# Kernel tuning notes

Hardware: AMD Instinct MI355X
Metric: run time of the kernel (lower is better)

## Reference

```python
import jax, jax.numpy as jnp
import numpy as np

EMBED_DIM = 1024
NUM_HEADS = 16
HEAD_DIM = EMBED_DIM // NUM_HEADS


def setup_inputs() -> dict:
    key = jax.random.key(0)
    ks = jax.random.split(key, 10)
    s = 1.0 / np.sqrt(EMBED_DIM)
    inp = {
        "x1": jax.random.normal(ks[0], (4, 1024, EMBED_DIM), jnp.float32),
        "x2": jax.random.normal(ks[1], (4, 2048, EMBED_DIM), jnp.float32),
        "Wq": jax.random.normal(ks[2], (EMBED_DIM, EMBED_DIM), jnp.float32) * s,
        "bq": jnp.zeros((EMBED_DIM,), jnp.float32),
        "Wk": jax.random.normal(ks[3], (EMBED_DIM, EMBED_DIM), jnp.float32) * s,
        "bk": jnp.zeros((EMBED_DIM,), jnp.float32),
        "Wv": jax.random.normal(ks[4], (EMBED_DIM, EMBED_DIM), jnp.float32) * s,
        "bv": jnp.zeros((EMBED_DIM,), jnp.float32),
        "Wo": jax.random.normal(ks[5], (EMBED_DIM, EMBED_DIM), jnp.float32) * s,
        "bo": jnp.zeros((EMBED_DIM,), jnp.float32),
    }
    return inp


def reference(x1, x2, Wq, bq, Wk, bk, Wv, bv, Wo, bo):
    B, Sq, E = x1.shape
    Skv = x2.shape[1]
    H, D = NUM_HEADS, HEAD_DIM
    # linear projections (PyTorch Linear: x @ W.T + b)
    q = (x1 @ Wq.T + bq).reshape(B, Sq, H, D).transpose(0, 2, 1, 3)   # [B,H,Sq,D]
    k = (x2 @ Wk.T + bk).reshape(B, Skv, H, D).transpose(0, 2, 1, 3)  # [B,H,Skv,D]
    v = (x2 @ Wv.T + bv).reshape(B, Skv, H, D).transpose(0, 2, 1, 3)
    scores = jnp.einsum("bhqd,bhkd->bhqk", q, k) / jnp.sqrt(jnp.float32(D))
    attn = jax.nn.softmax(scores, axis=-1)
    out = jnp.einsum("bhqk,bhkd->bhqd", attn, v)
    out = out.transpose(0, 2, 1, 3).reshape(B, Sq, E)
    return out @ Wo.T + bo
```

## Files before the change

kernel.cpp:

```cpp
#include <hip/hip_runtime.h>

typedef __attribute__((ext_vector_type(8))) short short8;
typedef __attribute__((ext_vector_type(4))) short short4v;
typedef __attribute__((ext_vector_type(4))) float f32x4;
typedef _Float16 half8 __attribute__((ext_vector_type(8)));

#define ASYNC16(g, l) __builtin_amdgcn_global_load_lds( \
    (__attribute__((address_space(1))) void*)(g), \
    (__attribute__((address_space(3))) void*)(l), 16, 0, 0)

__device__ __forceinline__ short f2bf(float f) {
  union { float f; unsigned u; } v; v.f = f;
  unsigned r = v.u + 0x7fffu + ((v.u >> 16) & 1u);
  return (short)(r >> 16);
}

__device__ __forceinline__ short f2h(float f) {
  _Float16 h = (_Float16)f;
  return __builtin_bit_cast(short, h);
}

__device__ __forceinline__ unsigned pkh2(float a, float b) {
  return __builtin_bit_cast(unsigned, __builtin_amdgcn_cvt_pkrtz(a, b));
}

__device__ __forceinline__ f32x4 fzero4() {
  f32x4 z; z[0] = 0.f; z[1] = 0.f; z[2] = 0.f; z[3] = 0.f; return z;
}

__device__ __forceinline__ void wg_barrier() {
  asm volatile("s_waitcnt lgkmcnt(0)\n\ts_barrier" ::: "memory");
}

__device__ __forceinline__ void wait6_barrier() {
  asm volatile("s_waitcnt vmcnt(6)\n\ts_barrier" ::: "memory");
}
__device__ __forceinline__ void wait0_barrier() {
  asm volatile("s_waitcnt vmcnt(0)\n\ts_barrier" ::: "memory");
}

__global__ __launch_bounds__(256) void cvt_all(
    const float* __restrict__ x1, const float* __restrict__ x2,
    const float* __restrict__ wq, const float* __restrict__ wk,
    const float* __restrict__ wv, const float* __restrict__ wo,
    short* __restrict__ dst) {
  long e = ((long)blockIdx.x * 256 + threadIdx.x) * 4;
  const float* src; long loc;
  if (e < 4194304L)       { src = x1; loc = e; }
  else if (e < 12582912L) { src = x2; loc = e - 4194304L; }
  else if (e < 13631488L) { src = wq; loc = e - 12582912L; }
  else if (e < 14680064L) { src = wk; loc = e - 13631488L; }
  else if (e < 15728640L) { src = wv; loc = e - 14680064L; }
  else                    { src = wo; loc = e - 15728640L; }
  float4 v = *(const float4*)(src + loc);
  short4v o;
  o[0] = f2bf(v.x); o[1] = f2bf(v.y); o[2] = f2bf(v.z); o[3] = f2bf(v.w);
  *(short4v*)(dst + e) = o;
}

__global__ __launch_bounds__(256) void proj(
    const short* __restrict__ xb1, const short* __restrict__ xb2,
    const short* __restrict__ wqp, const short* __restrict__ wkp, const short* __restrict__ wvp,
    const float* __restrict__ bq, const float* __restrict__ bk, const float* __restrict__ bv,
    short* __restrict__ qb, short* __restrict__ kb, short* __restrict__ vb) {
  __shared__ short smem[16384];
  short* As = smem;
  short* Bs = smem + 4096;
  const int tid = threadIdx.x, w = tid >> 6, lane = tid & 63;
  const int quad = lane >> 4, col = lane & 15;
  const int waveM = (w >> 1) * 64, waveN = (w & 1) * 64;
  const int my = blockIdx.x, bn = blockIdx.y * 128;
  const short* A; const short* W; const float* bias; int mode, bm;
  if (my < 32)      { A = xb1; W = wqp; bias = bq; mode = 0; bm = my * 128; }
  else if (my < 96) { A = xb2; W = wkp; bias = bk; mode = 1; bm = (my - 32) * 128; }
  else              { A = xb2; W = wvp; bias = bv; mode = 2; bm = (my - 96) * 128; }

  f32x4 acc[4][4];
  for (int mi = 0; mi < 4; ++mi)
    for (int ni = 0; ni < 4; ++ni)
      acc[mi][ni] = fzero4();

  const int srow = w * 16 + (lane >> 2), scol = (lane & 3) * 8;
  const short* ga = A + (size_t)(bm + srow) * 1024 + scol;
  const short* gb = W + (size_t)(bn + srow) * 1024 + scol;
  short* lA = As + w * 512;
  short* lB = Bs + w * 512;

  for (int kk = 0; kk < 1024; kk += 32) {
    __syncthreads();
    ASYNC16(ga + kk,         lA);
    ASYNC16(ga + kk + 65536, lA + 2048);
    ASYNC16(gb + kk,         lB);
    ASYNC16(gb + kk + 65536, lB + 2048);
    __syncthreads();
    short8 af[4], bf[4];
    for (int mi = 0; mi < 4; ++mi)
      af[mi] = *(const short8*)(As + (waveM + mi * 16 + col) * 32 + quad * 8);
    for (int ni = 0; ni < 4; ++ni)
      bf[ni] = *(const short8*)(Bs + (waveN + ni * 16 + col) * 32 + quad * 8);
    for (int mi = 0; mi < 4; ++mi)
      for (int ni = 0; ni < 4; ++ni)
        acc[mi][ni] = __builtin_amdgcn_mfma_f32_16x16x32_bf16(af[mi], bf[ni], acc[mi][ni], 0, 0, 0);
  }

  __syncthreads();
  for (int ni = 0; ni < 4; ++ni) {
    int nn = waveN + ni * 16 + col;
    float bvl = bias[bn + nn];
    for (int mi = 0; mi < 4; ++mi) {
      int m0 = waveM + mi * 16 + quad * 4;
      for (int r = 0; r < 4; ++r) {
        int m = m0 + r;
        float val = acc[mi][ni][r] + bvl;
        short sv;
        if (mode == 0)      sv = f2bf(val * 0.18033688011112042f);
        else if (mode == 1) sv = f2bf(val);
        else                sv = f2h(val);
        smem[m * 128 + (nn ^ ((m & 15) << 3))] = sv;
      }
    }
  }
  __syncthreads();
  if (mode < 2) {
    const int S = (mode == 0) ? 1024 : 2048;
    short* outp = (mode == 0) ? qb : kb;
    const int bb = bm / S, s0 = bm & (S - 1), h0 = bn >> 6;
    for (int it = 0; it < 8; ++it) {
      int f = (it * 256 + tid) * 8;
      int hh = f >> 13, rem = f & 8191, m = rem >> 6, d = rem & 63;
      int nn = hh * 64 + d;
      short8 val = *(const short8*)&smem[m * 128 + (nn ^ ((m & 15) << 3))];
      *(short8*)(outp + ((((size_t)(bb * 16 + h0 + hh)) * S + s0 + m) * 64 + d)) = val;
    }
  } else {
    const int bb = bm >> 11, s0 = bm & 2047, kt0 = s0 >> 6, h0 = bn >> 6;
    for (int it = 0; it < 8; ++it) {
      int f = (it * 256 + tid) * 8;
      int hh = f >> 13, rem = f & 8191, ktl = rem >> 12, r3 = rem & 4095;
      int d = r3 >> 6, kvp0 = r3 & 63;
      int nn = hh * 64 + d;
      short8 val;
      for (int j = 0; j < 8; ++j) {
        int kvp = kvp0 + j;
        int kv = ((kvp & 3) << 4) | (kvp >> 2);
        int m = ktl * 64 + kv;
        val[j] = smem[m * 128 + (nn ^ ((m & 15) << 3))];
      }
      *(short8*)(vb + ((((size_t)(bb * 16 + h0 + hh)) * 32 + (kt0 + ktl)) * 4096) + d * 64 + kvp0) = val;
    }
  }
}

__global__ __launch_bounds__(256) void out_gemm(
    const short* __restrict__ A, const short* __restrict__ W,
    const float* __restrict__ bias, float* __restrict__ out) {
  __shared__ short smem[24576];
  const int tid = threadIdx.x, w = tid >> 6, lane = tid & 63;
  const int quad = lane >> 4, col = lane & 15;
  const int waveM = (w >> 1) * 64, waveN = (w & 1) * 32;
  const int bn = blockIdx.x * 64, bm = blockIdx.y * 128;

  f32x4 acc[4][2];
  for (int mi = 0; mi < 4; ++mi)
    for (int ni = 0; ni < 2; ++ni)
      acc[mi][ni] = fzero4();

  const int arow = w * 16 + (lane >> 2), ac = (lane & 3) * 8;
  const short* ga = A + (size_t)(bm + arow) * 1024 + ac;
  const short* gb = W + (size_t)(bn + (tid >> 2)) * 1024 + (tid & 3) * 8;

  auto stage = [&](int b, int kk) {
    short* base = smem + b * 12288;
    short* lA0 = base + w * 512;
    short* lA1 = base + 4096 + w * 512;
    short* lB0 = base + 8192 + w * 512;
    short* lB1 = base + 10240 + w * 512;
    ASYNC16(ga + kk,              lA0);
    ASYNC16(ga + kk + 65536,      lA0 + 2048);
    ASYNC16(ga + kk + 32,         lA1);
    ASYNC16(ga + kk + 32 + 65536, lA1 + 2048);
    ASYNC16(gb + kk,              lB0);
    ASYNC16(gb + kk + 32,         lB1);
  };
  auto compute = [&](int b) {
    const short* base = smem + b * 12288;
    for (int kh = 0; kh < 2; ++kh) {
      const short* Ash = base + kh * 4096;
      const short* Bsh = base + 8192 + kh * 2048;
      short8 af[4], bf[2];
      for (int mi = 0; mi < 4; ++mi)
        af[mi] = *(const short8*)(Ash + (waveM + mi * 16 + col) * 32 + quad * 8);
      for (int ni = 0; ni < 2; ++ni)
        bf[ni] = *(const short8*)(Bsh + (waveN + ni * 16 + col) * 32 + quad * 8);
      for (int mi = 0; mi < 4; ++mi)
        for (int ni = 0; ni < 2; ++ni)
          acc[mi][ni] = __builtin_amdgcn_mfma_f32_16x16x32_bf16(af[mi], bf[ni], acc[mi][ni], 0, 0, 0);
    }
  };

  stage(0, 0);
  stage(1, 64);
  for (int it = 0; it < 14; ++it) {
    wait6_barrier();
    compute(it & 1);
    wg_barrier();
    stage(it & 1, (it + 2) * 64);
  }
  wait6_barrier();
  compute(0);
  wait0_barrier();
  compute(1);

  for (int ni = 0; ni < 2; ++ni) {
    int n = bn + waveN + ni * 16 + col;
    float bvl = bias[n];
    for (int mi = 0; mi < 4; ++mi) {
      int m0 = bm + waveM + mi * 16 + quad * 4;
      for (int r = 0; r < 4; ++r)
        out[(size_t)(m0 + r) * 1024 + n] = acc[mi][ni][r] + bvl;
    }
  }
}

__global__ __launch_bounds__(256, 2) void attn(
    const short* __restrict__ Q, const short* __restrict__ K,
    const short* __restrict__ V, short* __restrict__ O) {
  __shared__ short Ks[128 * 72];
  __shared__ short Vs[80 * 136];
  __shared__ short Ps[128 * 136];
  const int tid = threadIdx.x, w = tid >> 6, lane = tid & 63;
  const int quad = lane >> 4, col = lane & 15;
  const int bh = blockIdx.x, qt = blockIdx.y;
  const int b = bh >> 4, h = bh & 15;
  const int qbase = w * 32;

  const short* qp = Q + ((size_t)bh * 1024 + qt * 128) * 64;
  const short* kp = K + (size_t)bh * 131072;
  const short* vp = V + (size_t)bh * 131072;

  short8 aq[2][2];
  for (int mi = 0; mi < 2; ++mi) {
    const short* qr = qp + (qbase + mi * 16 + col) * 64 + quad * 8;
    aq[mi][0] = *(const short8*)qr;
    aq[mi][1] = *(const short8*)(qr + 32);
  }

  f32x4 oa[2][5];
  for (int mi = 0; mi < 2; ++mi)
    for (int ni = 0; ni < 5; ++ni)
      oa[mi][ni] = fzero4();

  for (int i = tid; i < 16 * 136; i += 256)
    Vs[64 * 136 + i] = (i < 136) ? (short)0x3C00 : (short)0;

  const int krow = lane + (w >> 1) * 64, kch = (w & 1) * 32;
  const int vd = lane, vch = w & 1, vkh = (w >> 1) * 32;

  short8 kpre[4], vpre[4];
  {
    const short* kg = kp + krow * 64 + kch;
    const short* vg = vp + vch * 4096 + vd * 64 + vkh;
    for (int i = 0; i < 4; ++i) kpre[i] = *(const short8*)(kg + i * 8);
    for (int i = 0; i < 4; ++i) vpre[i] = *(const short8*)(vg + i * 8);
  }

  for (int kt = 0; kt < 16; ++kt) {
    wg_barrier();
    for (int i = 0; i < 4; ++i)
      *(short8*)&Ks[krow * 72 + kch + i * 8] = kpre[i];
    for (int i = 0; i < 4; ++i)
      *(short8*)&Vs[vd * 136 + vch * 64 + vkh + i * 8] = vpre[i];
    {
      int ktn = (kt < 15) ? kt + 1 : kt;
      const short* kg = kp + ktn * 8192 + krow * 64 + kch;
      const short* vg = vp + (2 * ktn + vch) * 4096 + vd * 64 + vkh;
      for (int i = 0; i < 4; ++i) kpre[i] = *(const short8*)(kg + i * 8);
      for (int i = 0; i < 4; ++i) vpre[i] = *(const short8*)(vg + i * 8);
    }
    wg_barrier();

    f32x4 sf[2][8];
    for (int nk = 0; nk < 8; ++nk) {
      short8 bk0 = *(const short8*)&Ks[(nk * 16 + col) * 72 + quad * 8];
      short8 bk1 = *(const short8*)&Ks[(nk * 16 + col) * 72 + 32 + quad * 8];
      f32x4 z0 = fzero4(), z1 = fzero4();
      z0 = __builtin_amdgcn_mfma_f32_16x16x32_bf16(aq[0][0], bk0, z0, 0, 0, 0);
      z0 = __builtin_amdgcn_mfma_f32_16x16x32_bf16(aq[0][1], bk1, z0, 0, 0, 0);
      z1 = __builtin_amdgcn_mfma_f32_16x16x32_bf16(aq[1][0], bk0, z1, 0, 0, 0);
      z1 = __builtin_amdgcn_mfma_f32_16x16x32_bf16(aq[1][1], bk1, z1, 0, 0, 0);
      sf[0][nk] = z0;
      sf[1][nk] = z1;
    }

    for (int mi = 0; mi < 2; ++mi)
      for (int nk = 0; nk < 8; ++nk)
        for (int r = 0; r < 4; ++r)
          sf[mi][nk][r] = __builtin_amdgcn_exp2f(sf[mi][nk][r]);
    for (int mi = 0; mi < 2; ++mi)
      for (int r = 0; r < 4; ++r) {
        int row = qbase + mi * 16 + quad * 4 + r;
        uint2 d0, d1;
        d0.x = pkh2(sf[mi][0][r], sf[mi][1][r]);
        d0.y = pkh2(sf[mi][2][r], sf[mi][3][r]);
        d1.x = pkh2(sf[mi][4][r], sf[mi][5][r]);
        d1.y = pkh2(sf[mi][6][r], sf[mi][7][r]);
        *(uint2*)&Ps[row * 136 + col * 4]      = d0;
        *(uint2*)&Ps[row * 136 + 64 + col * 4] = d1;
      }

    for (int ks = 0; ks < 4; ++ks) {
      int koff = ks * 32 + quad * 8;
      half8 ap0 = *(const half8*)&Ps[(qbase + col) * 136 + koff];
      half8 ap1 = *(const half8*)&Ps[(qbase + 16 + col) * 136 + koff];
      for (int ni = 0; ni < 5; ++ni) {
        half8 bv = *(const half8*)&Vs[(ni * 16 + col) * 136 + koff];
        oa[0][ni] = __builtin_amdgcn_mfma_f32_16x16x32_f16(ap0, bv, oa[0][ni], 0, 0, 0);
        oa[1][ni] = __builtin_amdgcn_mfma_f32_16x16x32_f16(ap1, bv, oa[1][ni], 0, 0, 0);
      }
    }
  }

  float inv[2][4];
  for (int mi = 0; mi < 2; ++mi)
    for (int r = 0; r < 4; ++r) {
      float s = __shfl(oa[mi][4][r], lane & 48);
      inv[mi][r] = 1.f / s;
    }
  __syncthreads();
  for (int mi = 0; mi < 2; ++mi)
    for (int ni = 0; ni < 4; ++ni)
      for (int r = 0; r < 4; ++r)
        Ps[(qbase + mi * 16 + quad * 4 + r) * 64 + ni * 16 + col] = f2bf(oa[mi][ni][r] * inv[mi][r]);
  __syncthreads();
  for (int it = 0; it < 4; ++it) {
    int f = (it * 256 + tid) * 8;
    int q = f >> 6, d = f & 63;
    short8 val = *(const short8*)&Ps[q * 64 + d];
    *(short8*)(O + ((size_t)(b * 1024 + qt * 128 + q)) * 1024 + h * 64 + d) = val;
  }
}

extern "C" void kernel_launch(void* const* d_in, const int* in_sizes, int n_in,
                              void* d_out, int out_size, void* d_ws, size_t ws_size,
                              hipStream_t stream) {
  const float* x1 = (const float*)d_in[0];
  const float* x2 = (const float*)d_in[1];
  const float* Wq = (const float*)d_in[2];
  const float* bq = (const float*)d_in[3];
  const float* Wk = (const float*)d_in[4];
  const float* bk = (const float*)d_in[5];
  const float* Wv = (const float*)d_in[6];
  const float* bv = (const float*)d_in[7];
  const float* Wo = (const float*)d_in[8];
  const float* bo = (const float*)d_in[9];

  char* ws = (char*)d_ws;
  short* xb1 = (short*)(ws + 0);
  short* xb2 = (short*)(ws + 8388608);
  short* wqb = (short*)(ws + 25165824);
  short* wkb = (short*)(ws + 27262976);
  short* wvb = (short*)(ws + 29360128);
  short* wob = (short*)(ws + 31457280);
  short* qb  = (short*)(ws + 33554432);
  short* kb  = (short*)(ws + 41943040);
  short* vb  = (short*)(ws + 58720256);
  short* ob  = (short*)(ws + 75497472);

  cvt_all<<<16384, 256, 0, stream>>>(x1, x2, Wq, Wk, Wv, Wo, (short*)ws);
  proj<<<dim3(160, 8), 256, 0, stream>>>(xb1, xb2, wqb, wkb, wvb, bq, bk, bv, qb, kb, vb);
  attn<<<dim3(64, 8), 256, 0, stream>>>(qb, kb, vb, ob);
  out_gemm<<<dim3(16, 32), 256, 0, stream>>>(ob, wob, bo, (float*)d_out);
}
```

Before: 238.7 us.

## Triple-buffer projection GEMM LDS loads and swizzle columns to avoid bank conflicts

The projection GEMM now stages K tiles into a three-slot LDS ring with async global-to-LDS loads issued two tiles ahead. It waits with vmcnt(4) plus a barrier, replacing the two __syncthreads per iteration, so global loads overlap with MFMA compute. It also XOR-swizzles the 16-byte column chunk on both the store and read side to reduce LDS bank conflicts on the fragment reads. LDS use rises from 32KB to 48KB per block, which may lower occupancy.

```diff
diff --git a/kernel.cpp b/kernel.cpp
--- a/kernel.cpp
+++ b/kernel.cpp
@@ -32,6 +32,9 @@
   asm volatile("s_waitcnt lgkmcnt(0)\n\ts_barrier" ::: "memory");
 }
 
+__device__ __forceinline__ void wait4_barrier() {
+  asm volatile("s_waitcnt vmcnt(4) lgkmcnt(0)\n\ts_barrier" ::: "memory");
+}
 __device__ __forceinline__ void wait6_barrier() {
   asm volatile("s_waitcnt vmcnt(6)\n\ts_barrier" ::: "memory");
 }
@@ -63,9 +66,7 @@
     const short* __restrict__ wqp, const short* __restrict__ wkp, const short* __restrict__ wvp,
     const float* __restrict__ bq, const float* __restrict__ bk, const float* __restrict__ bv,
     short* __restrict__ qb, short* __restrict__ kb, short* __restrict__ vb) {
-  __shared__ short smem[16384];
-  short* As = smem;
-  short* Bs = smem + 4096;
+  __shared__ short smem[24576];
   const int tid = threadIdx.x, w = tid >> 6, lane = tid & 63;
   const int quad = lane >> 4, col = lane & 15;
   const int waveM = (w >> 1) * 64, waveN = (w & 1) * 64;
@@ -80,30 +81,46 @@
     for (int ni = 0; ni < 4; ++ni)
       acc[mi][ni] = fzero4();
 
-  const int srow = w * 16 + (lane >> 2), scol = (lane & 3) * 8;
+  const int srow = w * 16 + (lane >> 2);
+  const int scol = ((lane & 3) ^ ((lane >> 3) & 3)) * 8;
   const short* ga = A + (size_t)(bm + srow) * 1024 + scol;
   const short* gb = W + (size_t)(bn + srow) * 1024 + scol;
-  short* lA = As + w * 512;
-  short* lB = Bs + w * 512;
-
-  for (int kk = 0; kk < 1024; kk += 32) {
-    __syncthreads();
+  const int csw = (col >> 1) & 3;
+
+  auto stage = [&](int kt) {
+    short* base = smem + (kt % 3) * 8192;
+    short* lA = base + w * 512;
+    short* lB = base + 4096 + w * 512;
+    const int kk = kt * 32;
     ASYNC16(ga + kk,         lA);
     ASYNC16(ga + kk + 65536, lA + 2048);
     ASYNC16(gb + kk,         lB);
     ASYNC16(gb + kk + 65536, lB + 2048);
-    __syncthreads();
+  };
+  auto compute = [&](int kt) {
+    const short* As_ = smem + (kt % 3) * 8192;
+    const short* Bs_ = As_ + 4096;
     short8 af[4], bf[4];
     for (int mi = 0; mi < 4; ++mi)
-      af[mi] = *(const short8*)(As + (waveM + mi * 16 + col) * 32 + quad * 8);
+      af[mi] = *(const short8*)(As_ + (waveM + mi * 16 + col) * 32 + (quad ^ csw) * 8);
     for (int ni = 0; ni < 4; ++ni)
-      bf[ni] = *(const short8*)(Bs + (waveN + ni * 16 + col) * 32 + quad * 8);
+      bf[ni] = *(const short8*)(Bs_ + (waveN + ni * 16 + col) * 32 + (quad ^ csw) * 8);
     for (int mi = 0; mi < 4; ++mi)
       for (int ni = 0; ni < 4; ++ni)
         acc[mi][ni] = __builtin_amdgcn_mfma_f32_16x16x32_bf16(af[mi], bf[ni], acc[mi][ni], 0, 0, 0);
-  }
-
+  };
+
+  stage(0);
+  stage(1);
+  for (int kt = 0; kt < 31; ++kt) {
+    wait4_barrier();
+    if (kt < 30) stage(kt + 2);
+    compute(kt);
+  }
+  wait0_barrier();
+  compute(31);
   __syncthreads();
+
   for (int ni = 0; ni < 4; ++ni) {
     int nn = waveN + ni * 16 + col;
     float bvl = bias[bn + nn];
```

Result: no change. 237.0 us (-0.7%).

## Triple-buffer projection GEMM LDS loads and swizzle tile layout

Applied to the files above, without the earlier changes.

Replaces the synchronous load-then-compute loop in the QKV projection kernel with a three-stage LDS ring buffer. Async global-to-LDS loads run two k-tiles ahead, and partial vmcnt waits let memory traffic overlap the MFMA work. It also XOR-swizzles the 16-byte column chunks in LDS to reduce bank conflicts on fragment reads. LDS use grows from 32KB to 48KB per block, which may reduce occupancy.

```diff
diff --git a/kernel.cpp b/kernel.cpp
--- a/kernel.cpp
+++ b/kernel.cpp
@@ -32,6 +32,9 @@
   asm volatile("s_waitcnt lgkmcnt(0)\n\ts_barrier" ::: "memory");
 }
 
+__device__ __forceinline__ void wait4_barrier() {
+  asm volatile("s_waitcnt vmcnt(4) lgkmcnt(0)\n\ts_barrier" ::: "memory");
+}
 __device__ __forceinline__ void wait6_barrier() {
   asm volatile("s_waitcnt vmcnt(6)\n\ts_barrier" ::: "memory");
 }
@@ -63,9 +66,7 @@
     const short* __restrict__ wqp, const short* __restrict__ wkp, const short* __restrict__ wvp,
     const float* __restrict__ bq, const float* __restrict__ bk, const float* __restrict__ bv,
     short* __restrict__ qb, short* __restrict__ kb, short* __restrict__ vb) {
-  __shared__ short smem[16384];
-  short* As = smem;
-  short* Bs = smem + 4096;
+  __shared__ short smem[24576];
   const int tid = threadIdx.x, w = tid >> 6, lane = tid & 63;
   const int quad = lane >> 4, col = lane & 15;
   const int waveM = (w >> 1) * 64, waveN = (w & 1) * 64;
@@ -80,30 +81,54 @@
     for (int ni = 0; ni < 4; ++ni)
       acc[mi][ni] = fzero4();
 
-  const int srow = w * 16 + (lane >> 2), scol = (lane & 3) * 8;
+  const int srow = w * 16 + (lane >> 2);
+  const int scol = ((lane & 3) ^ ((lane >> 3) & 3)) * 8;
   const short* ga = A + (size_t)(bm + srow) * 1024 + scol;
   const short* gb = W + (size_t)(bn + srow) * 1024 + scol;
-  short* lA = As + w * 512;
-  short* lB = Bs + w * 512;
-
-  for (int kk = 0; kk < 1024; kk += 32) {
-    __syncthreads();
-    ASYNC16(ga + kk,         lA);
-    ASYNC16(ga + kk + 65536, lA + 2048);
-    ASYNC16(gb + kk,         lB);
-    ASYNC16(gb + kk + 65536, lB + 2048);
-    __syncthreads();
-    short8 af[4], bf[4];
-    for (int mi = 0; mi < 4; ++mi)
-      af[mi] = *(const short8*)(As + (waveM + mi * 16 + col) * 32 + quad * 8);
-    for (int ni = 0; ni < 4; ++ni)
-      bf[ni] = *(const short8*)(Bs + (waveN + ni * 16 + col) * 32 + quad * 8);
-    for (int mi = 0; mi < 4; ++mi)
-      for (int ni = 0; ni < 4; ++ni)
-        acc[mi][ni] = __builtin_amdgcn_mfma_f32_16x16x32_bf16(af[mi], bf[ni], acc[mi][ni], 0, 0, 0);
-  }
-
+  const int csw = (col >> 1) & 3;
+
+  int aoff[4], boff[4];
+  for (int mi = 0; mi < 4; ++mi)
+    aoff[mi] = (waveM + mi * 16 + col) * 32 + (quad ^ csw) * 8;
+  for (int ni = 0; ni < 4; ++ni)
+    boff[ni] = 4096 + (waveN + ni * 16 + col) * 32 + (quad ^ csw) * 8;
+  short* const stA = smem + w * 512;
+  short* const stB = smem + 4096 + w * 512;
+
+#define PSTAGE(B, KK) do {                       \
+    ASYNC16(ga + (KK),         stA + (B) * 8192); \
+    ASYNC16(ga + (KK) + 65536, stA + (B) * 8192 + 2048); \
+    ASYNC16(gb + (KK),         stB + (B) * 8192); \
+    ASYNC16(gb + (KK) + 65536, stB + (B) * 8192 + 2048); \
+  } while (0)
+
+#define PCOMPUTE(B, KK) do {                     \
+    const short* base_ = smem + (B) * 8192;      \
+    short8 af[4], bf[4];                         \
+    for (int mi = 0; mi < 4; ++mi)               \
+      af[mi] = *(const short8*)(base_ + aoff[mi]); \
+    for (int ni = 0; ni < 4; ++ni)               \
+      bf[ni] = *(const short8*)(base_ + boff[ni]); \
+    for (int mi = 0; mi < 4; ++mi)               \
+      for (int ni = 0; ni < 4; ++ni)             \
+        acc[mi][ni] = __builtin_amdgcn_mfma_f32_16x16x32_bf16(af[mi], bf[ni], acc[mi][ni], 0, 0, 0); \
+  } while (0)
+
+  PSTAGE(0, 0);
+  PSTAGE(1, 32);
+#pragma unroll 1
+  for (int t = 0; t < 10; ++t) {
+    const int kk = t * 96;
+    wait4_barrier(); PSTAGE(2, kk + 64);  PCOMPUTE(0, kk);
+    wait4_barrier(); PSTAGE(0, kk + 96);  PCOMPUTE(1, kk + 32);
+    wait4_barrier(); PSTAGE(1, kk + 128); PCOMPUTE(2, kk + 64);
+  }
+  wait4_barrier();  PCOMPUTE(0, 960);
+  wait0_barrier();  PCOMPUTE(1, 992);
   __syncthreads();
+#undef PSTAGE
+#undef PCOMPUTE
+
   for (int ni = 0; ni < 4; ++ni) {
     int nn = waveN + ni * 16 + col;
     float bvl = bias[bn + nn];
```

Measured after the change: 235.1 us. No clear change (-1.5%).
